# Kernel optimization log

Measured on AMD Instinct MI355X. Metric: run time of the kernel, lower is better.

## Reference

```python
import jax, jax.numpy as jnp
import numpy as np

HEAD = 16
HEAD_DIM = 64
DIM = 1024
NEG = -1000000000.0


def setup_inputs() -> dict:
    key = jax.random.key(0)
    ks = jax.random.split(key, 8)
    B, S = 4, 2048
    s = 0.02
    return {
        "Q": jax.random.normal(ks[0], (B, S, DIM), dtype=jnp.float32),
        "K": jax.random.normal(ks[1], (B, S, DIM), dtype=jnp.float32),
        "V": jax.random.normal(ks[2], (B, S, DIM), dtype=jnp.float32),
        "Wq": jax.random.normal(ks[3], (HEAD * HEAD_DIM, DIM), dtype=jnp.float32) * s,
        "Wk": jax.random.normal(ks[4], (HEAD * HEAD_DIM, DIM), dtype=jnp.float32) * s,
        "Wv": jax.random.normal(ks[5], (HEAD * HEAD_DIM, DIM), dtype=jnp.float32) * s,
        "Wo": jax.random.normal(ks[6], (DIM, HEAD * HEAD_DIM), dtype=jnp.float32) * s,
        "bo": jax.random.normal(ks[7], (DIM,), dtype=jnp.float32) * s,
    }


def reference(Q, K, V, Wq, Wk, Wv, Wo, bo):
    B, S, _ = Q.shape
    # projections (nn.Linear: x @ W^T), split heads -> (b, h, t, d)
    def proj(x, W):
        return (x @ W.T).reshape(B, S, HEAD, HEAD_DIM).transpose(0, 2, 1, 3)
    q = proj(Q, Wq)
    k = proj(K, Wk)
    v = proj(V, Wv)
    scores = jnp.einsum("bhqd,bhkd->bhqk", q, k) / jnp.sqrt(jnp.float32(HEAD_DIM))
    causal = jnp.tril(jnp.ones((S, S), dtype=bool))
    scores = jnp.where(causal, scores, NEG)
    weights = jax.nn.softmax(scores, axis=-1)
    out = jnp.einsum("bhqk,bhkd->bhqd", weights, v)
    out = out.transpose(0, 2, 1, 3).reshape(B, S, HEAD * HEAD_DIM)
    out = out @ Wo.T + bo
    return out, weights
```

## Files before the change

kernel.cpp:

```cpp
#include <hip/hip_runtime.h>
#include <hip/hip_bf16.h>

typedef __hip_bfloat16 bf16;
typedef __attribute__((ext_vector_type(8))) short bf16x8;
typedef __attribute__((ext_vector_type(4))) float f32x4;

#define HEADS 16
#define HDIM  64
#define DIM   1024
#define SEQ   2048
#define BATCH 4
#define BS    (BATCH * SEQ)
#define SCALE 0.125f
#define CS    0.1803368801111f

#define EXP2F(x) __builtin_amdgcn_exp2f(x)
#define MFMA16(a, b, c) __builtin_amdgcn_mfma_f32_16x16x32_bf16(a, b, c, 0, 0, 0)

__device__ __forceinline__ void gload_lds16(const void* g, void* l) {
    __builtin_amdgcn_global_load_lds(
        (const __attribute__((address_space(1))) void*)g,
        (__attribute__((address_space(3))) void*)l, 16, 0, 0);
}

__device__ __forceinline__ void cvt8(const float* __restrict__ src, bf16* __restrict__ dst,
                                     size_t i)
{
    float4 f0 = *(const float4*)&src[i];
    float4 f1 = *(const float4*)&src[i + 4];
    union { bf16 h[8]; uint4 u; } pk;
    pk.h[0] = __float2bfloat16(f0.x); pk.h[1] = __float2bfloat16(f0.y);
    pk.h[2] = __float2bfloat16(f0.z); pk.h[3] = __float2bfloat16(f0.w);
    pk.h[4] = __float2bfloat16(f1.x); pk.h[5] = __float2bfloat16(f1.y);
    pk.h[6] = __float2bfloat16(f1.z); pk.h[7] = __float2bfloat16(f1.w);
    *(uint4*)&dst[i] = pk.u;
}

__global__ __launch_bounds__(256) void cvt_kernel(
    const float* __restrict__ Q, const float* __restrict__ K, const float* __restrict__ V,
    const float* __restrict__ Wq, const float* __restrict__ Wk, const float* __restrict__ Wv,
    bf16* __restrict__ xq, bf16* __restrict__ xk, bf16* __restrict__ xv,
    bf16* __restrict__ wq, bf16* __restrict__ wk, bf16* __restrict__ wv)
{
    const int seg = blockIdx.y;
    const float* src; bf16* dst; size_t n;
    switch (seg) {
        case 0: src = Q;  dst = xq; n = (size_t)BS * DIM;   break;
        case 1: src = K;  dst = xk; n = (size_t)BS * DIM;   break;
        case 2: src = V;  dst = xv; n = (size_t)BS * DIM;   break;
        case 3: src = Wq; dst = wq; n = (size_t)DIM * DIM;  break;
        case 4: src = Wk; dst = wk; n = (size_t)DIM * DIM;  break;
        default: src = Wv; dst = wv; n = (size_t)DIM * DIM; break;
    }
    size_t i = ((size_t)blockIdx.x * 256 + threadIdx.x) * 8;
    if (i >= n) return;
    cvt8(src, dst, i);
}

__global__ __launch_bounds__(256) void cvt_wo_kernel(
    const float* __restrict__ Wo, bf16* __restrict__ wo)
{
    size_t i = ((size_t)blockIdx.x * 256 + threadIdx.x) * 8;
    cvt8(Wo, wo, i);
}

__device__ __forceinline__ void mfma_core_1024(
    const bf16* __restrict__ A, const bf16* __restrict__ B,
    int m0, int n0, bf16* sA, f32x4 acc[4][4])
{
    const int tid = threadIdx.x, lane = tid & 63, wave = tid >> 6;
    const int l15 = lane & 15, lg = lane >> 4;
    const int wr = wave >> 1, wc = wave & 1;
    bf16* sB = sA + 16 * 512;

    const bf16* gsrc = (wave < 2) ? A : B;
    const int   gm0  = (wave < 2) ? m0 : n0;
    bf16*       sdst = (wave < 2) ? sA : sB;
    const int   wv2  = wave & 1;

#define STAGE(k0_) { \
    _Pragma("unroll") for (int u = 0; u < 8; ++u) { \
        const int c = wv2 * 8 + u; \
        const int mg = c >> 1, s = c & 1; \
        gload_lds16(gsrc + (size_t)(gm0 + mg * 16 + l15) * DIM + (k0_) + s * 32 + lg * 8, \
                    sdst + c * 512); \
    } }

    STAGE(0);
#pragma unroll 1
    for (int t = 0; t < DIM / 64; ++t) {
        __syncthreads();
#pragma unroll
        for (int s = 0; s < 2; ++s) {
            bf16x8 af[4], bfr[4];
#pragma unroll
            for (int i = 0; i < 4; ++i)
                af[i] = *(const bf16x8*)(sA + ((wr * 4 + i) * 2 + s) * 512 + lane * 8);
#pragma unroll
            for (int j = 0; j < 4; ++j)
                bfr[j] = *(const bf16x8*)(sB + ((wc * 4 + j) * 2 + s) * 512 + lane * 8);
#pragma unroll
            for (int i = 0; i < 4; ++i)
#pragma unroll
                for (int j = 0; j < 4; ++j)
                    acc[i][j] = MFMA16(af[i], bfr[j], acc[i][j]);
        }
        __syncthreads();
        if (t < DIM / 64 - 1) STAGE((t + 1) * 64);
    }
#undef STAGE
}

__global__ __launch_bounds__(256) void proj_mfma_kernel(
    const bf16* __restrict__ Xq, const bf16* __restrict__ Xk, const bf16* __restrict__ Xv,
    const bf16* __restrict__ Wq, const bf16* __restrict__ Wk, const bf16* __restrict__ Wv,
    bf16* __restrict__ qo, bf16* __restrict__ ko, bf16* __restrict__ vo)
{
    __shared__ alignas(16) bf16 smem[16384];
    const int z = blockIdx.z;
    const bf16* X = z == 0 ? Xq : z == 1 ? Xk : Xv;
    const bf16* W = z == 0 ? Wq : z == 1 ? Wk : Wv;
    const int m0 = blockIdx.y * 128, n0 = blockIdx.x * 128;
    f32x4 acc[4][4] = {};
    mfma_core_1024(X, W, m0, n0, smem, acc);

    const int tid = threadIdx.x, lane = tid & 63, wave = tid >> 6;
    const int l15 = lane & 15, lg = lane >> 4, wr = wave >> 1, wc = wave & 1;
    const int h = blockIdx.x * 2 + wc;

    if (z != 2) {
        bf16* O = z == 0 ? qo : ko;
#pragma unroll
        for (int i = 0; i < 4; ++i)
#pragma unroll
            for (int r = 0; r < 4; ++r) {
                int m = m0 + wr * 64 + i * 16 + lg * 4 + r;
                int bb = m >> 11, ss = m & (SEQ - 1);
                size_t base = ((size_t)(bb * HEADS + h) * SEQ + ss) * HDIM;
#pragma unroll
                for (int j = 0; j < 4; ++j)
                    O[base + j * 16 + l15] = __float2bfloat16(acc[i][j][r]);
            }
    } else {
#pragma unroll
        for (int i = 0; i < 4; ++i) {
            int s0 = m0 + wr * 64 + i * 16 + lg * 4;
            int bb = s0 >> 11, ss = s0 & (SEQ - 1);
#pragma unroll
            for (int j = 0; j < 4; ++j) {
                int d = j * 16 + l15;
                union { bf16 h4[4]; uint2 u; } pk;
#pragma unroll
                for (int r = 0; r < 4; ++r) pk.h4[r] = __float2bfloat16(acc[i][j][r]);
                *(uint2*)&vo[((size_t)(bb * HEADS + h) * HDIM + d) * SEQ + ss] = pk.u;
            }
        }
    }
}

__global__ __launch_bounds__(256) void attn_kernel(
    const bf16* __restrict__ qws, const bf16* __restrict__ kws, const bf16* __restrict__ vtws,
    float* __restrict__ weights, bf16* __restrict__ attn_out)
{
    __shared__ alignas(16) bf16 Ks[4096];
    __shared__ alignas(16) bf16 Vs[4096];
    __shared__ alignas(16) bf16 Ps[4096];

    const int tid  = threadIdx.x;
    const int lane = tid & 63;
    const int wave = tid >> 6;
    const int l15  = lane & 15;
    const int lg   = lane >> 4;
    const int qt = (int)gridDim.x - 1 - (int)blockIdx.x;
    const int h  = blockIdx.y, b = blockIdx.z;
    const int bh = b * HEADS + h;
    const int q0 = qt * 64;
    const int qloc = 16 * wave + l15;

    const bf16* qbase = qws + (size_t)bh * SEQ * HDIM;
    const bf16* kbase = kws + (size_t)bh * SEQ * HDIM;
    const bf16* vbase = vtws + (size_t)bh * HDIM * SEQ;

    bf16x8 qa0, qa1;
    {
        const bf16* qp = qbase + (size_t)(q0 + qloc) * HDIM + lg * 8;
        qa0 = *(const bf16x8*)qp;
        qa1 = *(const bf16x8*)(qp + 32);
    }

#define LOADK(kt_, r0, r1) { \
    const bf16* rp = kbase + (size_t)((kt_) * 64 + 16 * wave + l15) * HDIM + lg * 8; \
    r0 = *(const uint4*)rp; r1 = *(const uint4*)(rp + 32); }
#define STOREK(r0, r1) { \
    *(uint4*)&Ks[((wave * 2 + 0) * 64 + lane) * 8] = r0; \
    *(uint4*)&Ks[((wave * 2 + 1) * 64 + lane) * 8] = r1; }
#define LOADV(kt_, r0, r1) { \
    const bf16* rp = vbase + (size_t)(16 * wave + l15) * SEQ + (kt_) * 64 + lg * 8; \
    r0 = *(const uint4*)rp; r1 = *(const uint4*)(rp + 32); }
#define STOREV(r0, r1) { \
    *(uint4*)&Vs[((wave * 2 + 0) * 64 + lane) * 8] = r0; \
    *(uint4*)&Vs[((wave * 2 + 1) * 64 + lane) * 8] = r1; }
#define QKT(acc_) { \
    _Pragma("unroll") \
    for (int ct = 0; ct < 4; ++ct) { \
        bf16x8 b0 = *(const bf16x8*)&Ks[((ct * 2 + 0) * 64 + lane) * 8]; \
        bf16x8 b1 = *(const bf16x8*)&Ks[((ct * 2 + 1) * 64 + lane) * 8]; \
        acc_[ct] = MFMA16(b0, qa0, acc_[ct]); \
        acc_[ct] = MFMA16(b1, qa1, acc_[ct]); \
    } }

    float m_run = -1e30f;
    float l_run = 0.f;

    {
        uint4 k0, k1;
        LOADK(0, k0, k1);
        STOREK(k0, k1);
    }
    for (int kt = 0; kt <= qt; ++kt) {
        __syncthreads();
        f32x4 acc[4] = {};
        QKT(acc);
        const bool more = kt < qt;
        uint4 nk0, nk1;
        if (more) LOADK(kt + 1, nk0, nk1);
        const bool diag = (kt == qt);
        float t[4][4];
#pragma unroll
        for (int ct = 0; ct < 4; ++ct)
#pragma unroll
            for (int r = 0; r < 4; ++r) {
                float v = acc[ct][r] * CS;
                if (diag && (ct * 16 + lg * 4 + r > qloc)) v = -1e30f;
                t[ct][r] = v;
            }
        float tm = -1e30f;
#pragma unroll
        for (int ct = 0; ct < 4; ++ct)
#pragma unroll
            for (int r = 0; r < 4; ++r) tm = fmaxf(tm, t[ct][r]);
        tm = fmaxf(tm, __shfl_xor(tm, 16));
        tm = fmaxf(tm, __shfl_xor(tm, 32));
        float mn = fmaxf(m_run, tm);
        float ps = 0.f;
#pragma unroll
        for (int ct = 0; ct < 4; ++ct)
#pragma unroll
            for (int r = 0; r < 4; ++r) ps += EXP2F(t[ct][r] - mn);
        ps += __shfl_xor(ps, 16);
        ps += __shfl_xor(ps, 32);
        l_run = l_run * EXP2F(m_run - mn) + ps;
        m_run = mn;
        __syncthreads();
        if (more) STOREK(nk0, nk1);
    }

    const float il = 1.0f / l_run;

    {
        uint4 k0, k1, v0, v1;
        LOADK(0, k0, k1);
        LOADV(0, v0, v1);
        STOREK(k0, k1);
        STOREV(v0, v1);
    }
    f32x4 oacc[4] = {};
    const size_t wrow = ((size_t)bh * SEQ + q0 + qloc) * SEQ;

    for (int kt = 0; kt <= qt; ++kt) {
        __syncthreads();
        f32x4 acc[4] = {};
        QKT(acc);
        const bool more = kt < qt;
        uint4 nk0, nk1, nv0, nv1;
        if (more) { LOADK(kt + 1, nk0, nk1); LOADV(kt + 1, nv0, nv1); }
        const bool diag = (kt == qt);
#pragma unroll
        for (int ct = 0; ct < 4; ++ct) {
            f32x4 w4;
            union { bf16 h4[4]; uint2 u; } pk;
#pragma unroll
            for (int r = 0; r < 4; ++r) {
                float v = acc[ct][r] * CS;
                if (diag && (ct * 16 + lg * 4 + r > qloc)) v = -1e30f;
                float w = EXP2F(v - m_run) * il;
                w4[r] = w;
                pk.h4[r] = __float2bfloat16(w);
            }
            __builtin_nontemporal_store(
                w4, (f32x4*)&weights[wrow + kt * 64 + ct * 16 + lg * 4]);
            *(uint2*)&Ps[(((wave * 2 + (ct >> 1)) * 64
                           + ((ct & 1) * 2 + (lg >> 1)) * 16 + l15) * 8
                          + (lg & 1) * 4)] = pk.u;
        }
        bf16x8 pa0 = *(const bf16x8*)&Ps[((wave * 2 + 0) * 64 + lane) * 8];
        bf16x8 pa1 = *(const bf16x8*)&Ps[((wave * 2 + 1) * 64 + lane) * 8];
#pragma unroll
        for (int td = 0; td < 4; ++td) {
            bf16x8 vb0 = *(const bf16x8*)&Vs[((td * 2 + 0) * 64 + lane) * 8];
            bf16x8 vb1 = *(const bf16x8*)&Vs[((td * 2 + 1) * 64 + lane) * 8];
            oacc[td] = MFMA16(pa0, vb0, oacc[td]);
            oacc[td] = MFMA16(pa1, vb1, oacc[td]);
        }
        __syncthreads();
        if (more) { STOREK(nk0, nk1); STOREV(nv0, nv1); }
    }

#pragma unroll
    for (int td = 0; td < 4; ++td)
#pragma unroll
        for (int r = 0; r < 4; ++r) {
            int rowg = q0 + 16 * wave + lg * 4 + r;
            attn_out[((size_t)b * SEQ + rowg) * DIM + h * HDIM + td * 16 + l15]
                = __float2bfloat16(oacc[td][r]);
        }

    const int zc0 = (qt + 1) * 64;
    if (zc0 < SEQ) {
        const int nc4 = (SEQ - zc0) >> 2;
        const size_t base = ((size_t)bh * SEQ + q0) * SEQ + zc0;
        const f32x4 z = {0.f, 0.f, 0.f, 0.f};
        for (int r = 0; r < 64; ++r)
            for (int c = tid; c < nc4; c += 256)
                __builtin_nontemporal_store(
                    z, (f32x4*)&weights[base + (size_t)r * SEQ + (size_t)c * 4]);
    }
#undef LOADK
#undef STOREK
#undef LOADV
#undef STOREV
#undef QKT
}

__global__ __launch_bounds__(256) void oproj_mfma_kernel(
    const bf16* __restrict__ A, const bf16* __restrict__ Wo,
    const float* __restrict__ bo, float* __restrict__ out)
{
    __shared__ alignas(16) bf16 smem[16384];
    const int m0 = blockIdx.y * 128, n0 = blockIdx.x * 128;
    f32x4 acc[4][4] = {};
    mfma_core_1024(A, Wo, m0, n0, smem, acc);

    const int tid = threadIdx.x, lane = tid & 63, wave = tid >> 6;
    const int l15 = lane & 15, lg = lane >> 4, wr = wave >> 1, wc = wave & 1;
    float bv[4];
#pragma unroll
    for (int j = 0; j < 4; ++j) bv[j] = bo[n0 + wc * 64 + j * 16 + l15];
#pragma unroll
    for (int i = 0; i < 4; ++i)
#pragma unroll
        for (int r = 0; r < 4; ++r) {
            int m = m0 + wr * 64 + i * 16 + lg * 4 + r;
#pragma unroll
            for (int j = 0; j < 4; ++j)
                out[(size_t)m * DIM + n0 + wc * 64 + j * 16 + l15] = acc[i][j][r] + bv[j];
        }
}

extern "C" void kernel_launch(void* const* d_in, const int* in_sizes, int n_in,
                              void* d_out, int out_size, void* d_ws, size_t ws_size,
                              hipStream_t stream)
{
    const float* Q  = (const float*)d_in[0];
    const float* K  = (const float*)d_in[1];
    const float* V  = (const float*)d_in[2];
    const float* Wq = (const float*)d_in[3];
    const float* Wk = (const float*)d_in[4];
    const float* Wv = (const float*)d_in[5];
    const float* Wo = (const float*)d_in[6];
    const float* bo = (const float*)d_in[7];

    float* out     = (float*)d_out;
    float* weights = out + (size_t)BS * DIM;

    const size_t XN = (size_t)BS * DIM;
    const size_t WN = (size_t)DIM * DIM;
    const size_t scratch_elems = 3 * XN + 3 * WN;
    bf16* cvt = (bf16*)(weights + ((size_t)268435456 - scratch_elems / 2));
    bf16* xq  = cvt;
    bf16* xk  = xq + XN;
    bf16* xv  = xk + XN;
    bf16* wqc = xv + XN;
    bf16* wkc = wqc + WN;
    bf16* wvc = wkc + WN;

    bf16* qws  = (bf16*)d_ws;
    bf16* kws  = qws + (size_t)BS * DIM;
    bf16* vtws = kws + (size_t)BS * DIM;
    bf16* aws  = vtws + (size_t)BS * DIM;
    bf16* woc  = qws;

    dim3 blk(256);
    cvt_kernel<<<dim3(4096, 6), blk, 0, stream>>>(
        Q, K, V, Wq, Wk, Wv, xq, xk, xv, wqc, wkc, wvc);
    proj_mfma_kernel<<<dim3(DIM / 128, BS / 128, 3), blk, 0, stream>>>(
        xq, xk, xv, wqc, wkc, wvc, qws, kws, vtws);
    attn_kernel<<<dim3(SEQ / 64, HEADS, BATCH), blk, 0, stream>>>(
        qws, kws, vtws, weights, aws);
    cvt_wo_kernel<<<dim3(WN / (256 * 8)), blk, 0, stream>>>(Wo, woc);
    oproj_mfma_kernel<<<dim3(DIM / 128, BS / 128), blk, 0, stream>>>(
        aws, woc, bo, out);
}
```

Baseline: 484.0 us.

## Enlarge attention query tile to 128 rows with 8 waves sharing K/V tiles

Raises the attention block from 64 to 128 query rows with 512 threads (8 waves). Each K/V tile staged in LDS is now reused by twice as many query rows, halving K/V reloads across blocks. Staging is split so waves 0-3 load K and waves 4-7 load V in the second pass. Waves whose rows lie entirely above a key tile skip compute and write zeros, which adds per-tile branching and halves the grid size.

```diff
diff --git a/kernel.cpp b/kernel.cpp
--- a/kernel.cpp
+++ b/kernel.cpp
@@ -13,6 +13,7 @@
 #define BS    (BATCH * SEQ)
 #define SCALE 0.125f
 #define CS    0.1803368801111f
+#define QBLK  128
 
 #define EXP2F(x) __builtin_amdgcn_exp2f(x)
 #define MFMA16(a, b, c) __builtin_amdgcn_mfma_f32_16x16x32_bf16(a, b, c, 0, 0, 0)
@@ -158,13 +159,13 @@
     }
 }
 
-__global__ __launch_bounds__(256) void attn_kernel(
+__global__ __launch_bounds__(512) void attn_kernel(
     const bf16* __restrict__ qws, const bf16* __restrict__ kws, const bf16* __restrict__ vtws,
     float* __restrict__ weights, bf16* __restrict__ attn_out)
 {
     __shared__ alignas(16) bf16 Ks[4096];
     __shared__ alignas(16) bf16 Vs[4096];
-    __shared__ alignas(16) bf16 Ps[4096];
+    __shared__ alignas(16) bf16 Ps[8192];
 
     const int tid  = threadIdx.x;
     const int lane = tid & 63;
@@ -174,12 +175,17 @@
     const int qt = (int)gridDim.x - 1 - (int)blockIdx.x;
     const int h  = blockIdx.y, b = blockIdx.z;
     const int bh = b * HEADS + h;
-    const int q0 = qt * 64;
+    const int q0 = qt * QBLK;
     const int qloc = 16 * wave + l15;
+    const int qmaxw = q0 + 16 * wave + 15;
+    const int nkt = 2 * qt + 2;
 
     const bf16* qbase = qws + (size_t)bh * SEQ * HDIM;
     const bf16* kbase = kws + (size_t)bh * SEQ * HDIM;
     const bf16* vbase = vtws + (size_t)bh * HDIM * SEQ;
+
+    const bool stagek = wave < 4;
+    const int  sw = wave & 3;
 
     bf16x8 qa0, qa1;
     {
@@ -189,17 +195,17 @@
     }
 
 #define LOADK(kt_, r0, r1) { \
-    const bf16* rp = kbase + (size_t)((kt_) * 64 + 16 * wave + l15) * HDIM + lg * 8; \
+    const bf16* rp = kbase + (size_t)((kt_) * 64 + 16 * sw + l15) * HDIM + lg * 8; \
     r0 = *(const uint4*)rp; r1 = *(const uint4*)(rp + 32); }
 #define STOREK(r0, r1) { \
-    *(uint4*)&Ks[((wave * 2 + 0) * 64 + lane) * 8] = r0; \
-    *(uint4*)&Ks[((wave * 2 + 1) * 64 + lane) * 8] = r1; }
+    *(uint4*)&Ks[((sw * 2 + 0) * 64 + lane) * 8] = r0; \
+    *(uint4*)&Ks[((sw * 2 + 1) * 64 + lane) * 8] = r1; }
 #define LOADV(kt_, r0, r1) { \
-    const bf16* rp = vbase + (size_t)(16 * wave + l15) * SEQ + (kt_) * 64 + lg * 8; \
+    const bf16* rp = vbase + (size_t)(16 * sw + l15) * SEQ + (kt_) * 64 + lg * 8; \
     r0 = *(const uint4*)rp; r1 = *(const uint4*)(rp + 32); }
 #define STOREV(r0, r1) { \
-    *(uint4*)&Vs[((wave * 2 + 0) * 64 + lane) * 8] = r0; \
-    *(uint4*)&Vs[((wave * 2 + 1) * 64 + lane) * 8] = r1; }
+    *(uint4*)&Vs[((sw * 2 + 0) * 64 + lane) * 8] = r0; \
+    *(uint4*)&Vs[((sw * 2 + 1) * 64 + lane) * 8] = r1; }
 #define QKT(acc_) { \
     _Pragma("unroll") \
     for (int ct = 0; ct < 4; ++ct) { \
@@ -212,98 +218,115 @@
     float m_run = -1e30f;
     float l_run = 0.f;
 
-    {
+    if (stagek) {
         uint4 k0, k1;
         LOADK(0, k0, k1);
         STOREK(k0, k1);
     }
-    for (int kt = 0; kt <= qt; ++kt) {
-        __syncthreads();
-        f32x4 acc[4] = {};
-        QKT(acc);
-        const bool more = kt < qt;
+    for (int kt = 0; kt < nkt; ++kt) {
+        __syncthreads();
+        const bool active = (kt * 64 <= qmaxw);
+        const bool more = kt + 1 < nkt;
         uint4 nk0, nk1;
-        if (more) LOADK(kt + 1, nk0, nk1);
-        const bool diag = (kt == qt);
-        float t[4][4];
-#pragma unroll
-        for (int ct = 0; ct < 4; ++ct)
-#pragma unroll
-            for (int r = 0; r < 4; ++r) {
-                float v = acc[ct][r] * CS;
-                if (diag && (ct * 16 + lg * 4 + r > qloc)) v = -1e30f;
-                t[ct][r] = v;
-            }
-        float tm = -1e30f;
-#pragma unroll
-        for (int ct = 0; ct < 4; ++ct)
-#pragma unroll
-            for (int r = 0; r < 4; ++r) tm = fmaxf(tm, t[ct][r]);
-        tm = fmaxf(tm, __shfl_xor(tm, 16));
-        tm = fmaxf(tm, __shfl_xor(tm, 32));
-        float mn = fmaxf(m_run, tm);
-        float ps = 0.f;
-#pragma unroll
-        for (int ct = 0; ct < 4; ++ct)
-#pragma unroll
-            for (int r = 0; r < 4; ++r) ps += EXP2F(t[ct][r] - mn);
-        ps += __shfl_xor(ps, 16);
-        ps += __shfl_xor(ps, 32);
-        l_run = l_run * EXP2F(m_run - mn) + ps;
-        m_run = mn;
-        __syncthreads();
-        if (more) STOREK(nk0, nk1);
+        if (active) {
+            f32x4 acc[4] = {};
+            QKT(acc);
+            if (stagek && more) LOADK(kt + 1, nk0, nk1);
+            const bool diag = (kt * 64 + 63 > qmaxw - 15);
+            float t[4][4];
+#pragma unroll
+            for (int ct = 0; ct < 4; ++ct)
+#pragma unroll
+                for (int r = 0; r < 4; ++r) {
+                    float v = acc[ct][r] * CS;
+                    if (diag && (kt * 64 + ct * 16 + lg * 4 + r > q0 + qloc)) v = -1e30f;
+                    t[ct][r] = v;
+                }
+            float tm = -1e30f;
+#pragma unroll
+            for (int ct = 0; ct < 4; ++ct)
+#pragma unroll
+                for (int r = 0; r < 4; ++r) tm = fmaxf(tm, t[ct][r]);
+            tm = fmaxf(tm, __shfl_xor(tm, 16));
+            tm = fmaxf(tm, __shfl_xor(tm, 32));
+            float mn = fmaxf(m_run, tm);
+            float ps = 0.f;
+#pragma unroll
+            for (int ct = 0; ct < 4; ++ct)
+#pragma unroll
+                for (int r = 0; r < 4; ++r) ps += EXP2F(t[ct][r] - mn);
+            ps += __shfl_xor(ps, 16);
+            ps += __shfl_xor(ps, 32);
+            l_run = l_run * EXP2F(m_run - mn) + ps;
+            m_run = mn;
+        } else {
+            if (stagek && more) LOADK(kt + 1, nk0, nk1);
+        }
+        __syncthreads();
+        if (stagek && more) STOREK(nk0, nk1);
     }
 
     const float il = 1.0f / l_run;
 
-    {
-        uint4 k0, k1, v0, v1;
+    if (stagek) {
+        uint4 k0, k1;
         LOADK(0, k0, k1);
+        STOREK(k0, k1);
+    } else {
+        uint4 v0, v1;
         LOADV(0, v0, v1);
-        STOREK(k0, k1);
         STOREV(v0, v1);
     }
     f32x4 oacc[4] = {};
     const size_t wrow = ((size_t)bh * SEQ + q0 + qloc) * SEQ;
 
-    for (int kt = 0; kt <= qt; ++kt) {
-        __syncthreads();
-        f32x4 acc[4] = {};
-        QKT(acc);
-        const bool more = kt < qt;
-        uint4 nk0, nk1, nv0, nv1;
-        if (more) { LOADK(kt + 1, nk0, nk1); LOADV(kt + 1, nv0, nv1); }
-        const bool diag = (kt == qt);
-#pragma unroll
-        for (int ct = 0; ct < 4; ++ct) {
-            f32x4 w4;
-            union { bf16 h4[4]; uint2 u; } pk;
-#pragma unroll
-            for (int r = 0; r < 4; ++r) {
-                float v = acc[ct][r] * CS;
-                if (diag && (ct * 16 + lg * 4 + r > qloc)) v = -1e30f;
-                float w = EXP2F(v - m_run) * il;
-                w4[r] = w;
-                pk.h4[r] = __float2bfloat16(w);
+    for (int kt = 0; kt < nkt; ++kt) {
+        __syncthreads();
+        const bool active = (kt * 64 <= qmaxw);
+        const bool more = kt + 1 < nkt;
+        uint4 n0, n1;
+        if (active) {
+            f32x4 acc[4] = {};
+            QKT(acc);
+            if (more) { if (stagek) LOADK(kt + 1, n0, n1) else LOADV(kt + 1, n0, n1) }
+            const bool diag = (kt * 64 + 63 > qmaxw - 15);
+#pragma unroll
+            for (int ct = 0; ct < 4; ++ct) {
+                f32x4 w4;
+                union { bf16 h4[4]; uint2 u; } pk;
+#pragma unroll
+                for (int r = 0; r < 4; ++r) {
+                    float v = acc[ct][r] * CS;
+                    if (diag && (kt * 64 + ct * 16 + lg * 4 + r > q0 + qloc)) v = -1e30f;
+                    float w = EXP2F(v - m_run) * il;
+                    w4[r] = w;
+                    pk.h4[r] = __float2bfloat16(w);
+                }
+                __builtin_nontemporal_store(
+                    w4, (f32x4*)&weights[wrow + kt * 64 + ct * 16 + lg * 4]);
+                *(uint2*)&Ps[wave * 1024
+                             + (((ct >> 1) * 64 + ((ct & 1) * 2 + (lg >> 1)) * 16 + l15) * 8
+                                + (lg & 1) * 4)] = pk.u;
             }
-            __builtin_nontemporal_store(
-                w4, (f32x4*)&weights[wrow + kt * 64 + ct * 16 + lg * 4]);
-            *(uint2*)&Ps[(((wave * 2 + (ct >> 1)) * 64
-                           + ((ct & 1) * 2 + (lg >> 1)) * 16 + l15) * 8
-                          + (lg & 1) * 4)] = pk.u;
-        }
-        bf16x8 pa0 = *(const bf16x8*)&Ps[((wave * 2 + 0) * 64 + lane) * 8];
-        bf16x8 pa1 = *(const bf16x8*)&Ps[((wave * 2 + 1) * 64 + lane) * 8];
-#pragma unroll
-        for (int td = 0; td < 4; ++td) {
-            bf16x8 vb0 = *(const bf16x8*)&Vs[((td * 2 + 0) * 64 + lane) * 8];
-            bf16x8 vb1 = *(const bf16x8*)&Vs[((td * 2 + 1) * 64 + lane) * 8];
-            oacc[td] = MFMA16(pa0, vb0, oacc[td]);
-            oacc[td] = MFMA16(pa1, vb1, oacc[td]);
-        }
-        __syncthreads();
-        if (more) { STOREK(nk0, nk1); STOREV(nv0, nv1); }
+            bf16x8 pa0 = *(const bf16x8*)&Ps[wave * 1024 + lane * 8];
+            bf16x8 pa1 = *(const bf16x8*)&Ps[wave * 1024 + 512 + lane * 8];
+#pragma unroll
+            for (int td = 0; td < 4; ++td) {
+                bf16x8 vb0 = *(const bf16x8*)&Vs[((td * 2 + 0) * 64 + lane) * 8];
+                bf16x8 vb1 = *(const bf16x8*)&Vs[((td * 2 + 1) * 64 + lane) * 8];
+                oacc[td] = MFMA16(pa0, vb0, oacc[td]);
+                oacc[td] = MFMA16(pa1, vb1, oacc[td]);
+            }
+        } else {
+            if (more) { if (stagek) LOADK(kt + 1, n0, n1) else LOADV(kt + 1, n0, n1) }
+            const f32x4 z = {0.f, 0.f, 0.f, 0.f};
+#pragma unroll
+            for (int ct = 0; ct < 4; ++ct)
+                __builtin_nontemporal_store(
+                    z, (f32x4*)&weights[wrow + kt * 64 + ct * 16 + lg * 4]);
+        }
+        __syncthreads();
+        if (more) { if (stagek) STOREK(n0, n1) else STOREV(n0, n1) }
     }
 
 #pragma unroll
@@ -315,13 +338,13 @@
                 = __float2bfloat16(oacc[td][r]);
         }
 
-    const int zc0 = (qt + 1) * 64;
+    const int zc0 = (qt + 1) * QBLK;
     if (zc0 < SEQ) {
         const int nc4 = (SEQ - zc0) >> 2;
         const size_t base = ((size_t)bh * SEQ + q0) * SEQ + zc0;
         const f32x4 z = {0.f, 0.f, 0.f, 0.f};
-        for (int r = 0; r < 64; ++r)
-            for (int c = tid; c < nc4; c += 256)
+        for (int r = 0; r < QBLK; ++r)
+            for (int c = tid; c < nc4; c += 512)
                 __builtin_nontemporal_store(
                     z, (f32x4*)&weights[base + (size_t)r * SEQ + (size_t)c * 4]);
     }
@@ -395,7 +418,7 @@
         Q, K, V, Wq, Wk, Wv, xq, xk, xv, wqc, wkc, wvc);
     proj_mfma_kernel<<<dim3(DIM / 128, BS / 128, 3), blk, 0, stream>>>(
         xq, xk, xv, wqc, wkc, wvc, qws, kws, vtws);
-    attn_kernel<<<dim3(SEQ / 64, HEADS, BATCH), blk, 0, stream>>>(
+    attn_kernel<<<dim3(SEQ / QBLK, HEADS, BATCH), dim3(512), 0, stream>>>(
         qws, kws, vtws, weights, aws);
     cvt_wo_kernel<<<dim3(WN / (256 * 8)), blk, 0, stream>>>(Wo, woc);
     oproj_mfma_kernel<<<dim3(DIM / 128, BS / 128), blk, 0, stream>>>(
```

New measurement: 525.7 us. 8.6% more time.
